# Kernel optimization log

Hardware: AMD Instinct MI355X
Metric: run time of the kernel (lower is better)

## Reference

```python
import jax, jax.numpy as jnp
import numpy as np

N = 50000      # nodes
D = 16         # regular in/out degree
E = N * D      # edges
IN_N = 128     # input node feature size
IN_E = 64      # input edge feature size
H = 64         # internal_size
H2 = 2 * H     # LSTM input/hidden size
OUT_N = 128
OUT_E = 64


def setup_inputs() -> dict:
    key = jax.random.key(0)
    ks = jax.random.split(key, 24)
    s = 0.05
    inp = {}
    inp["node_vecs"] = jax.random.normal(ks[0], (N, IN_N), jnp.float32)
    inp["edge_vecs"] = jax.random.normal(ks[1], (E, IN_E), jnp.float32)
    # ring digraph: edge e = i*D + k connects i -> (i+k+1) % N
    j = np.arange(N)[:, None]
    k = np.arange(D)[None, :]
    pni = (j - (k + 1)) % N
    inp["pred_node_idx"] = jnp.asarray(pni, jnp.int32)
    inp["pred_edge_idx"] = jnp.asarray(pni * D + k, jnp.int32)
    inp["succ_node_idx"] = jnp.asarray((j + k + 1) % N, jnp.int32)
    inp["succ_edge_idx"] = jnp.asarray(j * D + k, jnp.int32)
    src = np.repeat(np.arange(N), D)
    dst = (src + np.tile(np.arange(1, D + 1), N)) % N
    inp["edge_src"] = jnp.asarray(src, jnp.int32)
    inp["edge_dst"] = jnp.asarray(dst, jnp.int32)
    # parameters (torch Linear convention: y = x @ W.T + b)
    inp["Wn"] = jax.random.normal(ks[2], (H, IN_N), jnp.float32) * s
    inp["bn"] = jax.random.normal(ks[3], (H,), jnp.float32) * s
    inp["We"] = jax.random.normal(ks[4], (H, IN_E), jnp.float32) * s
    inp["be"] = jax.random.normal(ks[5], (H,), jnp.float32) * s
    # two LSTM aggregators (pred / succ), gate order i,f,g,o
    inp["Wih_p"] = jax.random.normal(ks[6], (4 * H2, H2), jnp.float32) * s
    inp["Whh_p"] = jax.random.normal(ks[7], (4 * H2, H2), jnp.float32) * s
    inp["bih_p"] = jax.random.normal(ks[8], (4 * H2,), jnp.float32) * s
    inp["bhh_p"] = jax.random.normal(ks[9], (4 * H2,), jnp.float32) * s
    inp["Wr_p"] = jax.random.normal(ks[10], (H, H2), jnp.float32) * s
    inp["br_p"] = jax.random.normal(ks[11], (H,), jnp.float32) * s
    inp["Wih_s"] = jax.random.normal(ks[12], (4 * H2, H2), jnp.float32) * s
    inp["Whh_s"] = jax.random.normal(ks[13], (4 * H2, H2), jnp.float32) * s
    inp["bih_s"] = jax.random.normal(ks[14], (4 * H2,), jnp.float32) * s
    inp["bhh_s"] = jax.random.normal(ks[15], (4 * H2,), jnp.float32) * s
    inp["Wr_s"] = jax.random.normal(ks[16], (H, H2), jnp.float32) * s
    inp["br_s"] = jax.random.normal(ks[17], (H,), jnp.float32) * s
    inp["Wt_n"] = jax.random.normal(ks[18], (OUT_N, 3 * H), jnp.float32) * s
    inp["bt_n"] = jax.random.normal(ks[19], (OUT_N,), jnp.float32) * s
    inp["Wt_e"] = jax.random.normal(ks[20], (OUT_E, 3 * H), jnp.float32) * s
    inp["bt_e"] = jax.random.normal(ks[21], (OUT_E,), jnp.float32) * s
    return inp


def _lstm_last(seq, Wih, Whh, bih, bhh):
    # seq: [N, D, 2H] -> last-timestep hidden state [N, 2H]
    n = seq.shape[0]
    h0 = jnp.zeros((n, H2), seq.dtype)

    def step(carry, x):
        h, c = carry
        g = x @ Wih.T + h @ Whh.T + (bih + bhh)
        i, f, gg, o = jnp.split(g, 4, axis=-1)
        c = jax.nn.sigmoid(f) * c + jax.nn.sigmoid(i) * jnp.tanh(gg)
        h = jax.nn.sigmoid(o) * jnp.tanh(c)
        return (h, c), None

    (h, _), _ = jax.lax.scan(step, (h0, h0), jnp.swapaxes(seq, 0, 1))
    return h


def _aggregate(hN, hE, nidx, eidx, Wih, Whh, bih, bhh, Wr, br):
    # gather neighbor sequences: concat(node pretrans, edge pretrans) -> [N, D, 2H]
    seq = jnp.concatenate([hN[nidx], hE[eidx]], axis=-1)
    h_last = _lstm_last(seq, Wih, Whh, bih, bhh)
    return jax.nn.relu(jax.nn.relu(h_last) @ Wr.T + br)  # [N, H]


def reference(node_vecs, edge_vecs, pred_node_idx, pred_edge_idx,
              succ_node_idx, succ_edge_idx, edge_src, edge_dst,
              Wn, bn, We, be,
              Wih_p, Whh_p, bih_p, bhh_p, Wr_p, br_p,
              Wih_s, Whh_s, bih_s, bhh_s, Wr_s, br_s,
              Wt_n, bt_n, Wt_e, bt_e):
    hN = jax.nn.relu(node_vecs @ Wn.T + bn)   # [N, H] node pretrans
    hE = jax.nn.relu(edge_vecs @ We.T + be)   # [E, H] edge pretrans
    agg_p = _aggregate(hN, hE, pred_node_idx, pred_edge_idx,
                       Wih_p, Whh_p, bih_p, bhh_p, Wr_p, br_p)
    agg_s = _aggregate(hN, hE, succ_node_idx, succ_edge_idx,
                       Wih_s, Whh_s, bih_s, bhh_s, Wr_s, br_s)
    node_in = jnp.concatenate([agg_p, hN, agg_s], axis=-1)      # [N, 3H]
    node_out = jax.nn.relu(node_in @ Wt_n.T + bt_n)             # [N, OUT_N]
    edge_in = jnp.concatenate([hN[edge_src], hE, hN[edge_dst]], axis=-1)  # [E, 3H]
    edge_out = jax.nn.relu(edge_in @ Wt_e.T + bt_e)             # [E, OUT_E]
    return node_out, edge_out
```

## Files before the change

### kernel.cpp

```cpp
#include <hip/hip_runtime.h>

#define DEV __device__ __forceinline__

typedef __bf16 bf16x8 __attribute__((ext_vector_type(8)));
typedef float floatx4 __attribute__((ext_vector_type(4)));
typedef unsigned short u16;

constexpr int NN    = 50000;
constexpr int DEG   = 16;
constexpr int H2    = 128;

constexpr size_t WS_WN    = 0;
constexpr size_t WS_WE    = 16384;
constexpr size_t WS_WIH_P = 24576;
constexpr size_t WS_WHH_P = 155648;
constexpr size_t WS_WR_P  = 286720;
constexpr size_t WS_WIH_S = 303104;
constexpr size_t WS_WHH_S = 434176;
constexpr size_t WS_WR_S  = 565248;
constexpr size_t WS_WT_N  = 581632;
constexpr size_t WS_WT_E  = 630784;
constexpr size_t WS_BSUM_P= 655360;
constexpr size_t WS_BSUM_S= 657408;
constexpr size_t WS_HN    = 659456;
constexpr size_t WS_AGGP  = 7059456;
constexpr size_t WS_AGGS  = 13459456;

DEV u16 f2bf(float x) {
  unsigned u = __builtin_bit_cast(unsigned, x);
  return (u16)((u + 0x7fffu + ((u >> 16) & 1u)) >> 16);
}
DEV bf16x8 ld8(const u16* p) { return *reinterpret_cast<const bf16x8*>(p); }
DEV floatx4 mfma16(bf16x8 a, bf16x8 b, floatx4 c) {
  return __builtin_amdgcn_mfma_f32_16x16x32_bf16(a, b, c, 0, 0, 0);
}
DEV floatx4 make4(float b) { floatx4 r = {b, b, b, b}; return r; }
DEV float sigf(float x) { return __builtin_amdgcn_rcpf(1.0f + __expf(-x)); }
DEV float tanhb(float x) {
  float e = __expf(-2.0f * x);
  return __builtin_fmaf(2.0f, __builtin_amdgcn_rcpf(1.0f + e), -1.0f);
}
DEV bf16x8 relu8(bf16x8 a) {
  typedef u16 u16x8 __attribute__((ext_vector_type(8)));
  u16x8 u = __builtin_bit_cast(u16x8, a);
#pragma unroll
  for (int i = 0; i < 8; ++i) u[i] = (u[i] & 0x8000u) ? (u16)0 : u[i];
  return __builtin_bit_cast(bf16x8, u);
}

__global__ void k_prep(const float* Wn, const float* We,
                       const float* WihP, const float* WhhP, const float* WrP,
                       const float* WihS, const float* WhhS, const float* WrS,
                       const float* WtN, const float* WtE,
                       const float* bihP, const float* bhhP,
                       const float* bihS, const float* bhhS,
                       u16* wbf, float* bsumP, float* bsumS) {
  int idx = blockIdx.x * blockDim.x + threadIdx.x;
  if (idx < 327680) {
    const float* src; int rel;
    if      (idx <   8192) { src = Wn;   rel = idx; }
    else if (idx <  12288) { src = We;   rel = idx - 8192; }
    else if (idx <  77824) { src = WihP; rel = idx - 12288; }
    else if (idx < 143360) { src = WhhP; rel = idx - 77824; }
    else if (idx < 151552) { src = WrP;  rel = idx - 143360; }
    else if (idx < 217088) { src = WihS; rel = idx - 151552; }
    else if (idx < 282624) { src = WhhS; rel = idx - 217088; }
    else if (idx < 290816) { src = WrS;  rel = idx - 282624; }
    else if (idx < 315392) { src = WtN;  rel = idx - 290816; }
    else                   { src = WtE;  rel = idx - 315392; }
    wbf[idx] = f2bf(src[rel]);
  } else if (idx < 328704) {
    int j = idx - 327680;
    if (j < 512) bsumP[j] = bihP[j] + bhhP[j];
    else         bsumS[j - 512] = bihS[j - 512] + bhhS[j - 512];
  }
}

__global__ __launch_bounds__(256, 4) void k_pre_node(const float* xv, const float* bias,
                                                     const u16* Wbf, u16* outbf) {
  __shared__ __align__(16) u16 Xs[64 * 136];
  const int tid = threadIdx.x;
  const int base = blockIdx.x * 64;
#pragma unroll
  for (int j = 0; j < 8; ++j) {
    int flat = tid + j * 256;
    int row = flat >> 5, c4 = flat & 31;
    int gr = base + row; if (gr >= NN) gr = NN - 1;
    float4 v = reinterpret_cast<const float4*>(xv + (size_t)gr * 128)[c4];
    ushort4 h; h.x = f2bf(v.x); h.y = f2bf(v.y); h.z = f2bf(v.z); h.w = f2bf(v.w);
    *reinterpret_cast<ushort4*>(&Xs[row * 136 + c4 * 4]) = h;
  }
  __syncthreads();
  const int wave = tid >> 6, lane = tid & 63, l16 = lane & 15, quad = lane >> 4;
  const int rt = wave;
  floatx4 acc[4];
#pragma unroll
  for (int ct = 0; ct < 4; ++ct) acc[ct] = make4(bias[ct * 16 + l16]);
#pragma unroll
  for (int kt = 0; kt < 4; ++kt) {
    bf16x8 a = ld8(&Xs[(rt * 16 + l16) * 136 + kt * 32 + quad * 8]);
#pragma unroll
    for (int ct = 0; ct < 4; ++ct) {
      bf16x8 b = ld8(Wbf + (ct * 16 + l16) * 128 + kt * 32 + quad * 8);
      acc[ct] = mfma16(a, b, acc[ct]);
    }
  }
#pragma unroll
  for (int ct = 0; ct < 4; ++ct)
#pragma unroll
    for (int r = 0; r < 4; ++r) {
      int row = base + rt * 16 + quad * 4 + r;
      if (row < NN) {
        float v = acc[ct][r]; v = v > 0.0f ? v : 0.0f;
        outbf[(size_t)row * 64 + ct * 16 + l16] = f2bf(v);
      }
    }
}

__global__ __launch_bounds__(256, 4) void k_pre_edge(const float* xv, const float* bias,
                                                     const u16* Wbf, u16* outbf) {
  __shared__ __align__(16) u16 Xs[64 * 72];
  const int tid = threadIdx.x;
  const size_t base = (size_t)blockIdx.x * 64;
#pragma unroll
  for (int j = 0; j < 4; ++j) {
    int flat = tid + j * 256;
    int row = flat >> 4, c4 = flat & 15;
    float4 v = reinterpret_cast<const float4*>(xv + (base + row) * 64)[c4];
    ushort4 h; h.x = f2bf(v.x); h.y = f2bf(v.y); h.z = f2bf(v.z); h.w = f2bf(v.w);
    *reinterpret_cast<ushort4*>(&Xs[row * 72 + c4 * 4]) = h;
  }
  __syncthreads();
  const int wave = tid >> 6, lane = tid & 63, l16 = lane & 15, quad = lane >> 4;
  const int rt = wave;
  floatx4 acc[4];
#pragma unroll
  for (int ct = 0; ct < 4; ++ct) acc[ct] = make4(bias[ct * 16 + l16]);
#pragma unroll
  for (int kt = 0; kt < 2; ++kt) {
    bf16x8 a = ld8(&Xs[(rt * 16 + l16) * 72 + kt * 32 + quad * 8]);
#pragma unroll
    for (int ct = 0; ct < 4; ++ct) {
      bf16x8 b = ld8(Wbf + (ct * 16 + l16) * 64 + kt * 32 + quad * 8);
      acc[ct] = mfma16(a, b, acc[ct]);
    }
  }
#pragma unroll
  for (int ct = 0; ct < 4; ++ct)
#pragma unroll
    for (int r = 0; r < 4; ++r) {
      size_t row = base + rt * 16 + quad * 4 + r;
      float v = acc[ct][r]; v = v > 0.0f ? v : 0.0f;
      outbf[row * 128 + ct * 16 + l16] = f2bf(v);
    }
}

__global__ __launch_bounds__(512, 2) void k_lstm(
    const u16* hN, const u16* hE,
    const int* nidxP, const int* eidxP, const int* nidxS, const int* eidxS,
    const u16* WihP, const u16* WhhP, const float* bsumP, const u16* WrP, const float* brP, u16* aggP,
    const u16* WihS, const u16* WhhS, const float* bsumS, const u16* WrS, const float* brS, u16* aggS) {
  __shared__ __align__(16) u16 Xs[2][32 * 136];
  __shared__ __align__(16) u16 Hs[2][32 * 136];
  __shared__ int nidx_s[512], eidx_s[512];

  const bool s = (blockIdx.y != 0);
  const int* nidx = s ? nidxS : nidxP;
  const int* eidx = s ? eidxS : eidxP;
  const u16* Wih = s ? WihS : WihP;
  const u16* Whh = s ? WhhS : WhhP;
  const float* bsum = s ? bsumS : bsumP;
  const u16* Wr = s ? WrS : WrP;
  const float* br = s ? brS : brP;
  u16* aggOut = s ? aggS : aggP;

  const int tid = threadIdx.x;
  const int base = blockIdx.x * 32;
  {
    int g = base * 16 + tid;
    int vn = 0, ve = 0;
    if (g < NN * 16) { vn = nidx[g]; ve = eidx[g]; }
    nidx_s[tid] = vn; eidx_s[tid] = ve;
  }
  for (int j = tid; j < 32 * 136 / 2; j += 512) reinterpret_cast<unsigned*>(Hs[0])[j] = 0u;

  const int wave = tid >> 6, lane = tid & 63, l16 = lane & 15, quad = lane >> 4;

  bf16x8 wx[4][4], wh[4][4];
  float bias[4];
#pragma unroll
  for (int g = 0; g < 4; ++g) {
    int gc = g * 128 + wave * 16 + l16;
    bias[g] = bsum[gc];
#pragma unroll
    for (int kt = 0; kt < 4; ++kt) {
      wx[g][kt] = ld8(Wih + gc * 128 + kt * 32 + quad * 8);
      wh[g][kt] = ld8(Whh + gc * 128 + kt * 32 + quad * 8);
    }
  }
  floatx4 cst[2] = {make4(0.0f), make4(0.0f)};
  __syncthreads();

  const int srow = tid >> 4, sub = tid & 15, seg = sub >> 3, soff = (sub & 7) * 8;
  const u16* sbase = seg ? hE : hN;
  const size_t sstride = seg ? 128 : 64;
  const int* sidx = seg ? eidx_s : nidx_s;

  {
    int r0 = sidx[srow * 16];
    uint4 v0 = *reinterpret_cast<const uint4*>(sbase + (size_t)r0 * sstride + soff);
    *reinterpret_cast<uint4*>(&Xs[0][srow * 136 + seg * 64 + soff]) = v0;
  }
  __syncthreads();

  for (int t = 0; t < DEG; ++t) {
    const int cur = t & 1, nxt = cur ^ 1;
    int tn = (t + 1 < DEG) ? (t + 1) : t;
    int rn = sidx[srow * 16 + tn];
    uint4 vnext = *reinterpret_cast<const uint4*>(sbase + (size_t)rn * sstride + soff);

    floatx4 acc[4][2];
#pragma unroll
    for (int g = 0; g < 4; ++g) { acc[g][0] = make4(bias[g]); acc[g][1] = make4(bias[g]); }
#pragma unroll
    for (int kt = 0; kt < 4; ++kt) {
      bf16x8 a0 = ld8(&Xs[cur][l16 * 136 + kt * 32 + quad * 8]);
#pragma unroll
      for (int g = 0; g < 4; ++g) acc[g][0] = mfma16(a0, wx[g][kt], acc[g][0]);
    }
#pragma unroll
    for (int kt = 0; kt < 4; ++kt) {
      bf16x8 h0 = ld8(&Hs[cur][l16 * 136 + kt * 32 + quad * 8]);
#pragma unroll
      for (int g = 0; g < 4; ++g) acc[g][0] = mfma16(h0, wh[g][kt], acc[g][0]);
    }
#pragma unroll
    for (int kt = 0; kt < 4; ++kt) {
      bf16x8 a1 = ld8(&Xs[cur][(16 + l16) * 136 + kt * 32 + quad * 8]);
#pragma unroll
      for (int g = 0; g < 4; ++g) acc[g][1] = mfma16(a1, wx[g][kt], acc[g][1]);
    }
#pragma unroll
    for (int kt = 0; kt < 4; ++kt) {
      bf16x8 h1 = ld8(&Hs[cur][(16 + l16) * 136 + kt * 32 + quad * 8]);
#pragma unroll
      for (int g = 0; g < 4; ++g) acc[g][1] = mfma16(h1, wh[g][kt], acc[g][1]);
    }

#pragma unroll
    for (int hh = 0; hh < 2; ++hh) {
#pragma unroll
      for (int rr = 0; rr < 4; ++rr) {
        float gi = acc[0][hh][rr], gf = acc[1][hh][rr];
        float gg = acc[2][hh][rr], go = acc[3][hh][rr];
        float c = sigf(gf) * cst[hh][rr] + sigf(gi) * tanhb(gg);
        float hv = sigf(go) * tanhb(c);
        cst[hh][rr] = c;
        Hs[nxt][(hh * 16 + quad * 4 + rr) * 136 + wave * 16 + l16] = f2bf(hv);
      }
    }

    if (t + 1 < DEG)
      *reinterpret_cast<uint4*>(&Xs[nxt][srow * 136 + seg * 64 + soff]) = vnext;
    __syncthreads();
  }

  {
    const int rt = wave >> 2, ct = wave & 3;
    floatx4 acc = make4(br[ct * 16 + l16]);
#pragma unroll
    for (int kt = 0; kt < 4; ++kt) {
      bf16x8 a = relu8(ld8(&Hs[0][(rt * 16 + l16) * 136 + kt * 32 + quad * 8]));
      bf16x8 b = ld8(Wr + (ct * 16 + l16) * 128 + kt * 32 + quad * 8);
      acc = mfma16(a, b, acc);
    }
#pragma unroll
    for (int rr = 0; rr < 4; ++rr) {
      int row = base + rt * 16 + quad * 4 + rr;
      if (row < NN) {
        float v = acc[rr] > 0.0f ? acc[rr] : 0.0f;
        aggOut[(size_t)row * 64 + ct * 16 + l16] = f2bf(v);
      }
    }
  }
}

__global__ __launch_bounds__(256, 4) void k_node_out(
    const u16* aggP, const u16* hN, const u16* aggS,
    const u16* Wt, const float* bt, float* outp) {
  __shared__ __align__(16) u16 Xs[64 * 200];
  const int tid = threadIdx.x;
  const int base = blockIdx.x * 64;
  const u16* segp[3] = {aggP, hN, aggS};
#pragma unroll
  for (int seg = 0; seg < 3; ++seg)
#pragma unroll
    for (int j = 0; j < 2; ++j) {
      int flat = tid + j * 256;
      int row = flat >> 3, off = (flat & 7) * 8;
      int gr = base + row; if (gr >= NN) gr = NN - 1;
      uint4 v = *reinterpret_cast<const uint4*>(segp[seg] + (size_t)gr * 64 + off);
      *reinterpret_cast<uint4*>(&Xs[row * 200 + seg * 64 + off]) = v;
    }
  __syncthreads();
  const int wave = tid >> 6, lane = tid & 63, l16 = lane & 15, quad = lane >> 4;
  const int rt = wave;
  floatx4 acc[8];
#pragma unroll
  for (int ct = 0; ct < 8; ++ct) acc[ct] = make4(bt[ct * 16 + l16]);
#pragma unroll
  for (int kt = 0; kt < 6; ++kt) {
    bf16x8 a = ld8(&Xs[(rt * 16 + l16) * 200 + kt * 32 + quad * 8]);
#pragma unroll
    for (int ct = 0; ct < 8; ++ct) {
      bf16x8 b = ld8(Wt + (ct * 16 + l16) * 192 + kt * 32 + quad * 8);
      acc[ct] = mfma16(a, b, acc[ct]);
    }
  }
#pragma unroll
  for (int ct = 0; ct < 8; ++ct)
#pragma unroll
    for (int r = 0; r < 4; ++r) {
      int row = base + rt * 16 + quad * 4 + r;
      if (row < NN) {
        float v = acc[ct][r];
        outp[(size_t)row * 128 + ct * 16 + l16] = v > 0.0f ? v : 0.0f;
      }
    }
}

__global__ __launch_bounds__(256, 4) void k_edge_out(
    const u16* hN, const u16* hE, const int* esrc, const int* edst,
    const u16* Wt, const float* bt, float* outp) {
  __shared__ __align__(16) u16 Xs[64 * 200];
  __shared__ int idxs[128];
  const int tid = threadIdx.x;
  const size_t base = (size_t)blockIdx.x * 64;
  if (tid < 64) idxs[tid] = esrc[base + tid];
  else if (tid < 128) idxs[tid] = edst[base + tid - 64];
  __syncthreads();
#pragma unroll
  for (int seg = 0; seg < 3; ++seg)
#pragma unroll
    for (int j = 0; j < 2; ++j) {
      int flat = tid + j * 256;
      int row = flat >> 3, off = (flat & 7) * 8;
      size_t grow;
      const u16* sp;
      if (seg == 0)      { grow = (size_t)idxs[row] * 64;       sp = hN; }
      else if (seg == 1) { grow = (base + row) * 128;           sp = hE; }
      else               { grow = (size_t)idxs[64 + row] * 64;  sp = hN; }
      uint4 v = *reinterpret_cast<const uint4*>(sp + grow + off);
      *reinterpret_cast<uint4*>(&Xs[row * 200 + seg * 64 + off]) = v;
    }
  __syncthreads();
  const int wave = tid >> 6, lane = tid & 63, l16 = lane & 15, quad = lane >> 4;
  const int rt = wave;
  floatx4 acc[4];
#pragma unroll
  for (int ct = 0; ct < 4; ++ct) acc[ct] = make4(bt[ct * 16 + l16]);
#pragma unroll
  for (int kt = 0; kt < 6; ++kt) {
    bf16x8 a = ld8(&Xs[(rt * 16 + l16) * 200 + kt * 32 + quad * 8]);
#pragma unroll
    for (int ct = 0; ct < 4; ++ct) {
      bf16x8 b = ld8(Wt + (ct * 16 + l16) * 192 + kt * 32 + quad * 8);
      acc[ct] = mfma16(a, b, acc[ct]);
    }
  }
#pragma unroll
  for (int ct = 0; ct < 4; ++ct)
#pragma unroll
    for (int r = 0; r < 4; ++r) {
      size_t row = base + rt * 16 + quad * 4 + r;
      float v = acc[ct][r];
      outp[row * 64 + ct * 16 + l16] = v > 0.0f ? v : 0.0f;
    }
}

extern "C" void kernel_launch(void* const* d_in, const int* in_sizes, int n_in,
                              void* d_out, int out_size, void* d_ws, size_t ws_size,
                              hipStream_t stream) {
  (void)in_sizes; (void)n_in; (void)out_size; (void)ws_size;
  const float* node_vecs = (const float*)d_in[0];
  const float* edge_vecs = (const float*)d_in[1];
  const int* pred_node_idx = (const int*)d_in[2];
  const int* pred_edge_idx = (const int*)d_in[3];
  const int* succ_node_idx = (const int*)d_in[4];
  const int* succ_edge_idx = (const int*)d_in[5];
  const int* edge_src = (const int*)d_in[6];
  const int* edge_dst = (const int*)d_in[7];
  const float* Wn = (const float*)d_in[8];
  const float* bn = (const float*)d_in[9];
  const float* We = (const float*)d_in[10];
  const float* be = (const float*)d_in[11];
  const float* Wih_p = (const float*)d_in[12];
  const float* Whh_p = (const float*)d_in[13];
  const float* bih_p = (const float*)d_in[14];
  const float* bhh_p = (const float*)d_in[15];
  const float* Wr_p = (const float*)d_in[16];
  const float* br_p = (const float*)d_in[17];
  const float* Wih_s = (const float*)d_in[18];
  const float* Whh_s = (const float*)d_in[19];
  const float* bih_s = (const float*)d_in[20];
  const float* bhh_s = (const float*)d_in[21];
  const float* Wr_s = (const float*)d_in[22];
  const float* br_s = (const float*)d_in[23];
  const float* Wt_n = (const float*)d_in[24];
  const float* bt_n = (const float*)d_in[25];
  const float* Wt_e = (const float*)d_in[26];
  const float* bt_e = (const float*)d_in[27];

  char* ws = (char*)d_ws;
  u16* wWn   = (u16*)(ws + WS_WN);
  u16* wWe   = (u16*)(ws + WS_WE);
  u16* wWihP = (u16*)(ws + WS_WIH_P);
  u16* wWhhP = (u16*)(ws + WS_WHH_P);
  u16* wWrP  = (u16*)(ws + WS_WR_P);
  u16* wWihS = (u16*)(ws + WS_WIH_S);
  u16* wWhhS = (u16*)(ws + WS_WHH_S);
  u16* wWrS  = (u16*)(ws + WS_WR_S);
  u16* wWtN  = (u16*)(ws + WS_WT_N);
  u16* wWtE  = (u16*)(ws + WS_WT_E);
  float* bsumP = (float*)(ws + WS_BSUM_P);
  float* bsumS = (float*)(ws + WS_BSUM_S);
  u16* hN   = (u16*)(ws + WS_HN);
  u16* aggP = (u16*)(ws + WS_AGGP);
  u16* aggS = (u16*)(ws + WS_AGGS);
  float* outN = (float*)d_out;
  float* outE = outN + (size_t)NN * 128;
  u16* hE = (u16*)outE;

  k_prep<<<1284, 256, 0, stream>>>(Wn, We, Wih_p, Whh_p, Wr_p, Wih_s, Whh_s, Wr_s,
                                   Wt_n, Wt_e, bih_p, bhh_p, bih_s, bhh_s,
                                   (u16*)ws, bsumP, bsumS);
  k_pre_node<<<782, 256, 0, stream>>>(node_vecs, bn, wWn, hN);
  k_pre_edge<<<12500, 256, 0, stream>>>(edge_vecs, be, wWe, hE);
  dim3 g3(1563, 2, 1);
  k_lstm<<<g3, 512, 0, stream>>>(hN, hE,
                                 pred_node_idx, pred_edge_idx, succ_node_idx, succ_edge_idx,
                                 wWihP, wWhhP, bsumP, wWrP, br_p, aggP,
                                 wWihS, wWhhS, bsumS, wWrS, br_s, aggS);
  k_node_out<<<782, 256, 0, stream>>>(aggP, hN, aggS, wWtN, bt_n, outN);
  k_edge_out<<<12500, 256, 0, stream>>>(hN, hE, edge_src, edge_dst, wWtE, bt_e, outE);
}
```

Before: 1.147 ms.

## Merge LSTM gate reciprocals, raise MFMA priority, use nontemporal output stores

Result: no change. 1.153 ms (+0.5%).

```diff
diff --git a/kernel.cpp b/kernel.cpp
--- a/kernel.cpp
+++ b/kernel.cpp
@@ -36,10 +36,7 @@
 }
 DEV floatx4 make4(float b) { floatx4 r = {b, b, b, b}; return r; }
 DEV float sigf(float x) { return __builtin_amdgcn_rcpf(1.0f + __expf(-x)); }
-DEV float tanhb(float x) {
-  float e = __expf(-2.0f * x);
-  return __builtin_fmaf(2.0f, __builtin_amdgcn_rcpf(1.0f + e), -1.0f);
-}
+DEV float expc(float x) { return __expf(fminf(x, 60.0f)); }
 DEV bf16x8 relu8(bf16x8 a) {
   typedef u16 u16x8 __attribute__((ext_vector_type(8)));
   u16x8 u = __builtin_bit_cast(u16x8, a);
@@ -222,6 +219,7 @@
     floatx4 acc[4][2];
 #pragma unroll
     for (int g = 0; g < 4; ++g) { acc[g][0] = make4(bias[g]); acc[g][1] = make4(bias[g]); }
+    __builtin_amdgcn_s_setprio(1);
 #pragma unroll
     for (int kt = 0; kt < 4; ++kt) {
       bf16x8 a0 = ld8(&Xs[cur][l16 * 136 + kt * 32 + quad * 8]);
@@ -246,17 +244,33 @@
 #pragma unroll
       for (int g = 0; g < 4; ++g) acc[g][1] = mfma16(h1, wh[g][kt], acc[g][1]);
     }
+    __builtin_amdgcn_s_setprio(0);
 
 #pragma unroll
     for (int hh = 0; hh < 2; ++hh) {
+      float hv[4];
 #pragma unroll
       for (int rr = 0; rr < 4; ++rr) {
         float gi = acc[0][hh][rr], gf = acc[1][hh][rr];
         float gg = acc[2][hh][rr], go = acc[3][hh][rr];
-        float c = sigf(gf) * cst[hh][rr] + sigf(gi) * tanhb(gg);
-        float hv = sigf(go) * tanhb(c);
+        float sf = sigf(gf);
+        float ei = __expf(-gi);
+        float eg = expc(-2.0f * gg);
+        float r1 = __builtin_amdgcn_rcpf((1.0f + ei) * (1.0f + eg));
+        float c  = __builtin_fmaf(sf, cst[hh][rr], (1.0f - eg) * r1);
         cst[hh][rr] = c;
-        Hs[nxt][(hh * 16 + quad * 4 + rr) * 136 + wave * 16 + l16] = f2bf(hv);
+        float eo = __expf(-go);
+        float ec = expc(-2.0f * c);
+        float r2 = __builtin_amdgcn_rcpf((1.0f + eo) * (1.0f + ec));
+        hv[rr] = (1.0f - ec) * r2;
+      }
+#pragma unroll
+      for (int rp = 0; rp < 2; ++rp) {
+        unsigned pk;
+        asm("v_cvt_pk_bf16_f32 %0, %1, %2" : "=v"(pk) : "v"(hv[rp * 2]), "v"(hv[rp * 2 + 1]));
+        const int r0 = hh * 16 + quad * 4 + rp * 2;
+        Hs[nxt][r0 * 136 + wave * 16 + l16] = (u16)pk;
+        Hs[nxt][(r0 + 1) * 136 + wave * 16 + l16] = (u16)(pk >> 16);
       }
     }
 
@@ -324,7 +338,8 @@
       int row = base + rt * 16 + quad * 4 + r;
       if (row < NN) {
         float v = acc[ct][r];
-        outp[(size_t)row * 128 + ct * 16 + l16] = v > 0.0f ? v : 0.0f;
+        __builtin_nontemporal_store(v > 0.0f ? v : 0.0f,
+                                    &outp[(size_t)row * 128 + ct * 16 + l16]);
       }
     }
 }
@@ -374,7 +389,8 @@
     for (int r = 0; r < 4; ++r) {
       size_t row = base + rt * 16 + quad * 4 + r;
       float v = acc[ct][r];
-      outp[row * 64 + ct * 16 + l16] = v > 0.0f ? v : 0.0f;
+      __builtin_nontemporal_store(v > 0.0f ? v : 0.0f,
+                                  &outp[row * 64 + ct * 16 + l16]);
     }
 }
 
```
